# Kernel tuning notes

Measured on AMD Instinct MI355X. Metric: run time of the kernel, lower is better.

## Reference

```python
import jax, jax.numpy as jnp
import numpy as np

N_HEAD = 16
MASK_NEG = -10000.0


def setup_inputs() -> dict:
    key = jax.random.key(0)
    k1, k2, k3 = jax.random.split(key, 3)
    B, S, D = 4, 2048, 1024
    x = jax.random.normal(k1, (B, S, D), dtype=jnp.float32)
    c_attn_w = jax.random.normal(k2, (D, 3 * D), dtype=jnp.float32) * 0.02
    c_attn_b = jnp.zeros((3 * D,), dtype=jnp.float32)
    c_proj_w = jax.random.normal(k3, (D, D), dtype=jnp.float32) * 0.02
    c_proj_b = jnp.zeros((D,), dtype=jnp.float32)
    return {"x": x, "c_attn_w": c_attn_w, "c_attn_b": c_attn_b,
            "c_proj_w": c_proj_w, "c_proj_b": c_proj_b}


def reference(x, c_attn_w, c_attn_b, c_proj_w, c_proj_b):
    B, S, D = x.shape
    H = N_HEAD
    Dh = D // H
    # fused QKV projection (Conv1D = x @ W + b)
    qkv = x @ c_attn_w + c_attn_b          # [B,S,3D]
    q, k, v = jnp.split(qkv, 3, axis=-1)   # each [B,S,D]
    # split heads -> [B,H,S,Dh]
    q = q.reshape(B, S, H, Dh).transpose(0, 2, 1, 3)
    k = k.reshape(B, S, H, Dh).transpose(0, 2, 1, 3)
    v = v.reshape(B, S, H, Dh).transpose(0, 2, 1, 3)
    # scores with scaling (scale=True)
    w = jnp.einsum('bhqd,bhkd->bhqk', q, k) / jnp.sqrt(jnp.float32(Dh))
    # multiplicative causal mask: w*b + -10000*(1-b)
    b = jnp.tril(jnp.ones((S, S), dtype=w.dtype))[None, None]  # [1,1,S,S]
    w = w * b + MASK_NEG * (1.0 - b)
    w = jax.nn.softmax(w, axis=-1)
    # dropout is identity at inference
    a = jnp.einsum('bhqk,bhkd->bhqd', w, v)  # [B,H,S,Dh]
    a = a.transpose(0, 2, 1, 3).reshape(B, S, D)  # merge heads
    out = a @ c_proj_w + c_proj_b
    return out
```

## Files before the change

kernel.cpp:

```cpp
#include <hip/hip_runtime.h>

typedef unsigned short u16;
typedef short bf16x8 __attribute__((ext_vector_type(8)));
typedef float f32x4 __attribute__((ext_vector_type(4)));
typedef unsigned int u32;
typedef u32 u32x4 __attribute__((ext_vector_type(4)));

#define B_ 4
#define S_ 2048
#define D_ 1024
#define H_ 16
#define DH_ 64
#define M_ 8192
#define SCL2E 0.1803368801111244f

__device__ __forceinline__ u16 f2b(float f) {
  union { float f; unsigned int u; } v; v.f = f;
  unsigned int u = v.u;
  unsigned int r = (u + 0x7FFFu + ((u >> 16) & 1u)) >> 16;
  return (u16)r;
}

__device__ __forceinline__ void gload16(const void* g, void* l) {
  __builtin_amdgcn_global_load_lds(
      (const __attribute__((address_space(1))) unsigned int*)g,
      (__attribute__((address_space(3))) unsigned int*)l,
      16, 0, 0);
}

__device__ __forceinline__ u32 cvt_pk_bf16(float lo, float hi) {
  u32 r;
  asm("v_cvt_pk_bf16_f32 %0, %1, %2" : "=v"(r) : "v"(lo), "v"(hi));
  return r;
}

struct __attribute__((aligned(8))) u16x4 { u16 x, y, z, w; };

__global__ __launch_bounds__(256) void prep_fused(
    const float* __restrict__ x, u16* __restrict__ xb,
    const float* __restrict__ w1, u16* __restrict__ w1t,
    const float* __restrict__ w2, u16* __restrict__ w2t) {
  __shared__ float tile[32][33];
  const int bid = blockIdx.x, t = threadIdx.x;

  if (bid < 2048) {
    const int n = M_ * D_;
    for (int i = (bid * 256 + t) * 4; i < n; i += 2048 * 256 * 4) {
      float4 v = *(const float4*)(x + i);
      u16x4 o; o.x = f2b(v.x); o.y = f2b(v.y); o.z = f2b(v.z); o.w = f2b(v.w);
      *(u16x4*)(xb + i) = o;
    }
    return;
  }

  const float* in;  u16* outp;  int R, C, bx, by;
  if (bid < 5120) {
    int rel = bid - 2048; bx = rel % 96; by = rel / 96;
    in = w1; outp = w1t; R = 1024; C = 3072;
  } else {
    int rel = bid - 5120; bx = rel % 32; by = rel / 32;
    in = w2; outp = w2t; R = 1024; C = 1024;
  }
  const int c0 = bx * 32, r0 = by * 32;
  const int tx = t & 31, ty = t >> 5;
#pragma unroll
  for (int j = 0; j < 32; j += 8)
    tile[ty + j][tx] = in[(size_t)(r0 + ty + j) * C + c0 + tx];
  __syncthreads();
#pragma unroll
  for (int j = 0; j < 32; j += 8)
    outp[(size_t)(c0 + ty + j) * R + r0 + tx] = f2b(tile[tx][ty + j]);
}

template <int MODE>
__global__ __launch_bounds__(256) void gemm_bt(
    const u16* __restrict__ A, const u16* __restrict__ BT,
    const float* __restrict__ bias, float* __restrict__ outf,
    u16* __restrict__ qb, u16* __restrict__ kb, u16* __restrict__ vtb,
    int Ncols, int Kdim) {
  __shared__ __attribute__((aligned(16))) u16 lsA[2][128 * 64];
  __shared__ __attribute__((aligned(16))) u16 lsB[2][128 * 64];
  const int t = threadIdx.x;
  const int lane = t & 63, w = t >> 6;
  const int lhi = lane >> 4, llo = lane & 15;

  const int gx = gridDim.x;
  const int lin = blockIdx.y * gx + blockIdx.x;
  const int nwg = gx * gridDim.y;
  const int sw = (lin & 7) * (nwg >> 3) + (lin >> 3);
  const int m0 = (sw / gx) * 128, n0 = (sw % gx) * 128;

  const int wr = (w >> 1) * 64, wc = (w & 1) * 64;

  const int r8 = lane >> 3;
  const int scolE = ((lane & 7) ^ r8) * 8;
  const int srow = w * 32 + r8;

  f32x4 acc[4][4] = {};
  const int nt = Kdim >> 6;

#define STAGE_G(buf, kk0)                                                        \
  _Pragma("unroll") for (int j = 0; j < 4; ++j) {                                \
    gload16(A + (size_t)(m0 + srow + j * 8) * Kdim + (kk0) + scolE,              \
            &lsA[buf][(w * 32 + j * 8) * 64]);                                   \
    gload16(BT + (size_t)(n0 + srow + j * 8) * Kdim + (kk0) + scolE,             \
            &lsB[buf][(w * 32 + j * 8) * 64]);                                   \
  }

  STAGE_G(0, 0)

  for (int tt = 0; tt < nt; ++tt) {
    const int cur = tt & 1;
    if (tt + 1 < nt) {
      STAGE_G(cur ^ 1, (tt + 1) << 6)
      asm volatile("s_waitcnt vmcnt(8)" ::: "memory");
    } else {
      asm volatile("s_waitcnt vmcnt(0)" ::: "memory");
    }
    __builtin_amdgcn_sched_barrier(0);
    __builtin_amdgcn_s_barrier();
    __builtin_amdgcn_sched_barrier(0);
#pragma unroll
    for (int kk = 0; kk < 2; ++kk) {
      bf16x8 af[4], bfr[4];
#pragma unroll
      for (int i = 0; i < 4; ++i) {
        int ra = wr + i * 16 + llo;
        af[i] = *(const bf16x8*)((const char*)&lsA[cur][ra * 64] +
                                 ((kk * 64 + lhi * 16) ^ ((ra & 7) << 4)));
        int rb = wc + i * 16 + llo;
        bfr[i] = *(const bf16x8*)((const char*)&lsB[cur][rb * 64] +
                                  ((kk * 64 + lhi * 16) ^ ((rb & 7) << 4)));
      }
#pragma unroll
      for (int mi = 0; mi < 4; ++mi)
#pragma unroll
        for (int ni = 0; ni < 4; ++ni)
          acc[mi][ni] = __builtin_amdgcn_mfma_f32_16x16x32_bf16(af[mi], bfr[ni], acc[mi][ni], 0, 0, 0);
    }
    __builtin_amdgcn_sched_barrier(0);
    __builtin_amdgcn_s_barrier();
  }
#undef STAGE_G

  if (MODE == 0) {
#pragma unroll
    for (int mi = 0; mi < 4; ++mi)
#pragma unroll
      for (int ni = 0; ni < 4; ++ni)
#pragma unroll
        for (int r = 0; r < 4; ++r) {
          int m = m0 + wr + mi * 16 + lhi * 4 + r;
          int n = n0 + wc + ni * 16 + llo;
          outf[(size_t)m * Ncols + n] = acc[mi][ni][r] + bias[n];
        }
  } else if (n0 < 1024) {
#pragma unroll
    for (int mi = 0; mi < 4; ++mi)
#pragma unroll
      for (int ni = 0; ni < 4; ++ni)
#pragma unroll
        for (int r = 0; r < 4; ++r) {
          int m = m0 + wr + mi * 16 + lhi * 4 + r;
          int n = n0 + wc + ni * 16 + llo;
          int bidx = m >> 11, s = m & 2047, hh = n >> 6, dh = n & 63;
          qb[((size_t)(bidx * 16 + hh) * 2048 + s) * 64 + dh] =
              f2b((acc[mi][ni][r] + bias[n]) * SCL2E);
        }
  } else if (n0 < 2048) {
#pragma unroll
    for (int mi = 0; mi < 4; ++mi)
#pragma unroll
      for (int ni = 0; ni < 4; ++ni)
#pragma unroll
        for (int r = 0; r < 4; ++r) {
          int m = m0 + wr + mi * 16 + lhi * 4 + r;
          int n2 = n0 - 1024 + wc + ni * 16 + llo;
          int bidx = m >> 11, s = m & 2047, hh = n2 >> 6, dh = n2 & 63;
          kb[((size_t)(bidx * 16 + hh) * 2048 + s) * 64 + dh] =
              f2b(acc[mi][ni][r] + bias[n0 + wc + ni * 16 + llo]);
        }
  } else {
#pragma unroll
    for (int mi = 0; mi < 4; ++mi)
#pragma unroll
      for (int ni = 0; ni < 4; ++ni)
#pragma unroll
        for (int r = 0; r < 4; ++r) {
          int m = m0 + wr + mi * 16 + lhi * 4 + r;
          int n2 = n0 - 2048 + wc + ni * 16 + llo;
          int bidx = m >> 11, s = m & 2047, hh = n2 >> 6, dh = n2 & 63;
          int col = (s & ~127) | ((s & 15) * 8 + ((s >> 4) & 7));
          vtb[((size_t)(bidx * 16 + hh) * 64 + dh) * 2048 + col] =
              f2b(acc[mi][ni][r] + bias[n0 + wc + ni * 16 + llo]);
        }
  }
}

__global__ __launch_bounds__(512) void attn128(
    const u16* __restrict__ Qb, const u16* __restrict__ Kb,
    const u16* __restrict__ VTb, u16* __restrict__ AO) {
  __shared__ __attribute__((aligned(16))) u16 kls[128 * 64];
  __shared__ __attribute__((aligned(16))) u16 vls[64 * 128];
  __shared__ __attribute__((aligned(16))) u16 pl[8][16][136];
  const int t = threadIdx.x, w = t >> 6, lane = t & 63;
  const int lhi = lane >> 4, llo = lane & 15;

  const int lin = blockIdx.y * 8 + blockIdx.x;
  const int bh = ((lin >> 6) << 3) | (lin & 7);
  const int pr = (lin >> 3) & 7;
  const int bb = bh >> 4, hh = bh & 15;

  const u16* Qp = Qb + (size_t)bh * (S_ * DH_);
  const u16* Kp = Kb + (size_t)bh * (S_ * DH_);
  const u16* Vp = VTb + (size_t)bh * (DH_ * S_);

  bf16x8 ones;
#pragma unroll
  for (int i = 0; i < 8; ++i) ones[i] = (short)0x3F80;

  int krow[2], kcolE[2], kdst[2], vrow[2], vcolE[2], vdst[2];
#pragma unroll
  for (int c = 0; c < 2; ++c) {
    int b = c * 8192 + t * 16;
    krow[c] = b >> 7;
    kcolE[c] = (b & 127) >> 1;
    kdst[c] = krow[c] * 128 + ((b & 127) ^ ((krow[c] & 7) << 4));
    vrow[c] = b >> 8;
    vcolE[c] = (b & 255) >> 1;
    vdst[c] = vrow[c] * 256 + ((b & 255) ^ ((vrow[c] & 15) << 4));
  }

  for (int ci = 0; ci < 2; ++ci) {
    const int qc = ci ? (15 - pr) : pr;
    const int q0 = qc * 128;
    const int qrow = q0 + w * 16 + llo;
    bf16x8 aq0 = *(const bf16x8*)(Qp + (size_t)qrow * DH_ + lhi * 8);
    bf16x8 aq1 = *(const bf16x8*)(Qp + (size_t)qrow * DH_ + 32 + lhi * 8);
    const int n128 = qc + 1;

    bf16x8 kst[2], vst[2];
#pragma unroll
    for (int c = 0; c < 2; ++c) {
      kst[c] = *(const bf16x8*)(Kp + (size_t)krow[c] * DH_ + kcolE[c]);
      vst[c] = *(const bf16x8*)(Vp + (size_t)vrow[c] * S_ + vcolE[c]);
    }
    __syncthreads();
#pragma unroll
    for (int c = 0; c < 2; ++c) {
      *(bf16x8*)((char*)kls + kdst[c]) = kst[c];
      *(bf16x8*)((char*)vls + vdst[c]) = vst[c];
    }
    __syncthreads();

    f32x4 o[4] = {};
    f32x4 osum = {};
    const int crow = q0 + w * 16 + lhi * 4;
    const int sw = (llo & 7) << 4;

    for (int tt = 0; tt < n128 - 1; ++tt) {
      const int kv0 = tt << 7;
#pragma unroll
      for (int c = 0; c < 2; ++c) {
        kst[c] = *(const bf16x8*)(Kp + (size_t)(kv0 + 128 + krow[c]) * DH_ + kcolE[c]);
        vst[c] = *(const bf16x8*)(Vp + (size_t)vrow[c] * S_ + kv0 + 128 + vcolE[c]);
      }

      f32x4 sc[8] = {};
      __builtin_amdgcn_s_setprio(1);
#pragma unroll
      for (int f = 0; f < 8; ++f) {
        const char* base = (const char*)kls + (f * 16 + llo) * 128;
        bf16x8 bk0 = *(const bf16x8*)(base + ((lhi * 16) ^ sw));
        bf16x8 bk1 = *(const bf16x8*)(base + ((64 + lhi * 16) ^ sw));
        sc[f] = __builtin_amdgcn_mfma_f32_16x16x32_bf16(aq0, bk0, sc[f], 0, 0, 0);
        sc[f] = __builtin_amdgcn_mfma_f32_16x16x32_bf16(aq1, bk1, sc[f], 0, 0, 0);
      }
      __builtin_amdgcn_s_setprio(0);

#pragma unroll
      for (int r = 0; r < 4; ++r) {
        float p[8];
#pragma unroll
        for (int f = 0; f < 8; ++f) p[f] = exp2f(sc[f][r]);
        u32x4 pw;
        pw[0] = cvt_pk_bf16(p[0], p[1]);
        pw[1] = cvt_pk_bf16(p[2], p[3]);
        pw[2] = cvt_pk_bf16(p[4], p[5]);
        pw[3] = cvt_pk_bf16(p[6], p[7]);
        *(u32x4*)((char*)&pl[w][lhi * 4 + r][0] + llo * 16) = pw;
      }

      __builtin_amdgcn_s_setprio(1);
#pragma unroll
      for (int kk = 0; kk < 4; ++kk) {
        bf16x8 ap = *(const bf16x8*)((const char*)&pl[w][llo][0] + kk * 64 + lhi * 16);
#pragma unroll
        for (int f = 0; f < 4; ++f) {
          const char* vbase = (const char*)vls + (f * 16 + llo) * 256;
          bf16x8 bv = *(const bf16x8*)(vbase + ((kk * 64 + lhi * 16) ^ (llo << 4)));
          o[f] = __builtin_amdgcn_mfma_f32_16x16x32_bf16(ap, bv, o[f], 0, 0, 0);
        }
        osum = __builtin_amdgcn_mfma_f32_16x16x32_bf16(ap, ones, osum, 0, 0, 0);
      }
      __builtin_amdgcn_s_setprio(0);

      __syncthreads();
#pragma unroll
      for (int c = 0; c < 2; ++c) {
        *(bf16x8*)((char*)kls + kdst[c]) = kst[c];
        *(bf16x8*)((char*)vls + vdst[c]) = vst[c];
      }
      __syncthreads();
    }

    {
      const int kv0 = (n128 - 1) << 7;
      f32x4 sc[8] = {};
      __builtin_amdgcn_s_setprio(1);
#pragma unroll
      for (int f = 0; f < 8; ++f) {
        const char* base = (const char*)kls + (f * 16 + llo) * 128;
        bf16x8 bk0 = *(const bf16x8*)(base + ((lhi * 16) ^ sw));
        bf16x8 bk1 = *(const bf16x8*)(base + ((64 + lhi * 16) ^ sw));
        sc[f] = __builtin_amdgcn_mfma_f32_16x16x32_bf16(aq0, bk0, sc[f], 0, 0, 0);
        sc[f] = __builtin_amdgcn_mfma_f32_16x16x32_bf16(aq1, bk1, sc[f], 0, 0, 0);
      }
      __builtin_amdgcn_s_setprio(0);

#pragma unroll
      for (int r = 0; r < 4; ++r) {
        float p[8];
#pragma unroll
        for (int f = 0; f < 8; ++f) {
          float x = sc[f][r];
          if (kv0 + f * 16 + llo > crow + r) x = -1e30f;
          p[f] = exp2f(x);
        }
        u32x4 pw;
        pw[0] = cvt_pk_bf16(p[0], p[1]);
        pw[1] = cvt_pk_bf16(p[2], p[3]);
        pw[2] = cvt_pk_bf16(p[4], p[5]);
        pw[3] = cvt_pk_bf16(p[6], p[7]);
        *(u32x4*)((char*)&pl[w][lhi * 4 + r][0] + llo * 16) = pw;
      }

      __builtin_amdgcn_s_setprio(1);
#pragma unroll
      for (int kk = 0; kk < 4; ++kk) {
        bf16x8 ap = *(const bf16x8*)((const char*)&pl[w][llo][0] + kk * 64 + lhi * 16);
#pragma unroll
        for (int f = 0; f < 4; ++f) {
          const char* vbase = (const char*)vls + (f * 16 + llo) * 256;
          bf16x8 bv = *(const bf16x8*)(vbase + ((kk * 64 + lhi * 16) ^ (llo << 4)));
          o[f] = __builtin_amdgcn_mfma_f32_16x16x32_bf16(ap, bv, o[f], 0, 0, 0);
        }
        osum = __builtin_amdgcn_mfma_f32_16x16x32_bf16(ap, ones, osum, 0, 0, 0);
      }
      __builtin_amdgcn_s_setprio(0);
    }

#pragma unroll
    for (int f = 0; f < 4; ++f)
#pragma unroll
      for (int r = 0; r < 4; ++r) {
        int row = crow + r;
        int dh = f * 16 + llo;
        float val = o[f][r] / osum[r];
        AO[((size_t)bb * S_ + row) * D_ + hh * DH_ + dh] = f2b(val);
      }
  }
}

extern "C" void kernel_launch(void* const* d_in, const int* in_sizes, int n_in,
                              void* d_out, int out_size, void* d_ws, size_t ws_size,
                              hipStream_t stream) {
  const float* x  = (const float*)d_in[0];
  const float* w1 = (const float*)d_in[1];
  const float* b1 = (const float*)d_in[2];
  const float* w2 = (const float*)d_in[3];
  const float* b2 = (const float*)d_in[4];
  float* out = (float*)d_out;
  char* ws = (char*)d_ws;

  u16* xb  = (u16*)(ws);
  u16* w1t = (u16*)(ws + 16777216);
  u16* w2t = (u16*)(ws + 23068672);
  u16* qb  = (u16*)(ws + 25165824);
  u16* kb  = (u16*)(ws + 41943040);
  u16* vtb = (u16*)(ws + 58720256);
  u16* ao  = xb;

  prep_fused<<<6144, 256, 0, stream>>>(x, xb, w1, w1t, w2, w2t);

  gemm_bt<1><<<dim3(24, 64), 256, 0, stream>>>(xb, w1t, b1, nullptr, qb, kb, vtb, 3072, 1024);
  attn128<<<dim3(8, 64), 512, 0, stream>>>(qb, kb, vtb, ao);
  gemm_bt<0><<<dim3(8, 64), 256, 0, stream>>>(ao, w2t, b2, out, nullptr, nullptr, nullptr, 1024, 1024);
}
```

Before: 182.4 us.

## Stage K/V into LDS via direct global-to-LDS loads with pre-swizzled global layout

The QKV GEMM epilogue now writes K and V^T in an XOR-swizzled order, so the attention kernel can copy tiles straight into LDS with global_load_lds instead of staging them through registers. K gets a double buffer so the next tile's load is issued right after the score MFMAs. The P scratch buffer loses its padding and uses an XOR swizzle instead, and exp2f is replaced by raw v_exp_f32. This removes register staging and VGPR pressure, but V is still single-buffered behind a barrier and v_exp_f32 skips denormal handling.

```diff
diff --git a/kernel.cpp b/kernel.cpp
--- a/kernel.cpp
+++ b/kernel.cpp
@@ -31,6 +31,12 @@
 __device__ __forceinline__ u32 cvt_pk_bf16(float lo, float hi) {
   u32 r;
   asm("v_cvt_pk_bf16_f32 %0, %1, %2" : "=v"(r) : "v"(lo), "v"(hi));
+  return r;
+}
+
+__device__ __forceinline__ float fexp2(float x) {
+  float r;
+  asm("v_exp_f32 %0, %1" : "=v"(r) : "v"(x));
   return r;
 }
 
@@ -176,7 +182,8 @@
         for (int r = 0; r < 4; ++r) {
           int m = m0 + wr + mi * 16 + lhi * 4 + r;
           int n2 = n0 - 1024 + wc + ni * 16 + llo;
-          int bidx = m >> 11, s = m & 2047, hh = n2 >> 6, dh = n2 & 63;
+          int bidx = m >> 11, s = m & 2047, hh = n2 >> 6;
+          int dh = (n2 & 63) ^ ((s & 7) << 3);
           kb[((size_t)(bidx * 16 + hh) * 2048 + s) * 64 + dh] =
               f2b(acc[mi][ni][r] + bias[n0 + wc + ni * 16 + llo]);
         }
@@ -190,7 +197,8 @@
           int m = m0 + wr + mi * 16 + lhi * 4 + r;
           int n2 = n0 - 2048 + wc + ni * 16 + llo;
           int bidx = m >> 11, s = m & 2047, hh = n2 >> 6, dh = n2 & 63;
-          int col = (s & ~127) | ((s & 15) * 8 + ((s >> 4) & 7));
+          int slot = (s & 15) * 8 + ((s >> 4) & 7);
+          int col = (s & ~127) | (slot ^ ((dh & 15) << 3));
           vtb[((size_t)(bidx * 16 + hh) * 64 + dh) * 2048 + col] =
               f2b(acc[mi][ni][r] + bias[n0 + wc + ni * 16 + llo]);
         }
@@ -200,9 +208,9 @@
 __global__ __launch_bounds__(512) void attn128(
     const u16* __restrict__ Qb, const u16* __restrict__ Kb,
     const u16* __restrict__ VTb, u16* __restrict__ AO) {
-  __shared__ __attribute__((aligned(16))) u16 kls[128 * 64];
+  __shared__ __attribute__((aligned(16))) u16 kls[2][128 * 64];
   __shared__ __attribute__((aligned(16))) u16 vls[64 * 128];
-  __shared__ __attribute__((aligned(16))) u16 pl[8][16][136];
+  __shared__ __attribute__((aligned(16))) u16 pl[8][16][128];
   const int t = threadIdx.x, w = t >> 6, lane = t & 63;
   const int lhi = lane >> 4, llo = lane & 15;
 
@@ -219,17 +227,15 @@
 #pragma unroll
   for (int i = 0; i < 8; ++i) ones[i] = (short)0x3F80;
 
-  int krow[2], kcolE[2], kdst[2], vrow[2], vcolE[2], vdst[2];
-#pragma unroll
-  for (int c = 0; c < 2; ++c) {
-    int b = c * 8192 + t * 16;
-    krow[c] = b >> 7;
-    kcolE[c] = (b & 127) >> 1;
-    kdst[c] = krow[c] * 128 + ((b & 127) ^ ((krow[c] & 7) << 4));
-    vrow[c] = b >> 8;
-    vcolE[c] = (b & 255) >> 1;
-    vdst[c] = vrow[c] * 256 + ((b & 255) ^ ((vrow[c] & 15) << 4));
-  }
+#define STAGE_K(buf, kv0) {                                           \
+    const u16* s_ = Kp + (size_t)(kv0) * 64 + t * 8;                  \
+    gload16(s_,        &kls[buf][w * 512]);                           \
+    gload16(s_ + 4096, &kls[buf][4096 + w * 512]); }
+#define STAGE_V(kv0) {                                                \
+    gload16(Vp + (size_t)(t >> 4) * S_ + (kv0) + (t & 15) * 8,        \
+            &vls[w * 512]);                                           \
+    gload16(Vp + (size_t)(32 + (t >> 4)) * S_ + (kv0) + (t & 15) * 8, \
+            &vls[4096 + w * 512]); }
 
   for (int ci = 0; ci < 2; ++ci) {
     const int qc = ci ? (15 - pr) : pr;
@@ -239,18 +245,9 @@
     bf16x8 aq1 = *(const bf16x8*)(Qp + (size_t)qrow * DH_ + 32 + lhi * 8);
     const int n128 = qc + 1;
 
-    bf16x8 kst[2], vst[2];
-#pragma unroll
-    for (int c = 0; c < 2; ++c) {
-      kst[c] = *(const bf16x8*)(Kp + (size_t)krow[c] * DH_ + kcolE[c]);
-      vst[c] = *(const bf16x8*)(Vp + (size_t)vrow[c] * S_ + vcolE[c]);
-    }
     __syncthreads();
-#pragma unroll
-    for (int c = 0; c < 2; ++c) {
-      *(bf16x8*)((char*)kls + kdst[c]) = kst[c];
-      *(bf16x8*)((char*)vls + vdst[c]) = vst[c];
-    }
+    STAGE_K(0, 0)
+    STAGE_V(0)
     __syncthreads();
 
     f32x4 o[4] = {};
@@ -260,17 +257,13 @@
 
     for (int tt = 0; tt < n128 - 1; ++tt) {
       const int kv0 = tt << 7;
-#pragma unroll
-      for (int c = 0; c < 2; ++c) {
-        kst[c] = *(const bf16x8*)(Kp + (size_t)(kv0 + 128 + krow[c]) * DH_ + kcolE[c]);
-        vst[c] = *(const bf16x8*)(Vp + (size_t)vrow[c] * S_ + kv0 + 128 + vcolE[c]);
-      }
+      const int cur = tt & 1;
 
       f32x4 sc[8] = {};
       __builtin_amdgcn_s_setprio(1);
 #pragma unroll
       for (int f = 0; f < 8; ++f) {
-        const char* base = (const char*)kls + (f * 16 + llo) * 128;
+        const char* base = (const char*)&kls[cur][0] + (f * 16 + llo) * 128;
         bf16x8 bk0 = *(const bf16x8*)(base + ((lhi * 16) ^ sw));
         bf16x8 bk1 = *(const bf16x8*)(base + ((64 + lhi * 16) ^ sw));
         sc[f] = __builtin_amdgcn_mfma_f32_16x16x32_bf16(aq0, bk0, sc[f], 0, 0, 0);
@@ -278,23 +271,27 @@
       }
       __builtin_amdgcn_s_setprio(0);
 
+      STAGE_K(cur ^ 1, kv0 + 128)
+
 #pragma unroll
       for (int r = 0; r < 4; ++r) {
         float p[8];
 #pragma unroll
-        for (int f = 0; f < 8; ++f) p[f] = exp2f(sc[f][r]);
+        for (int f = 0; f < 8; ++f) p[f] = fexp2(sc[f][r]);
         u32x4 pw;
         pw[0] = cvt_pk_bf16(p[0], p[1]);
         pw[1] = cvt_pk_bf16(p[2], p[3]);
         pw[2] = cvt_pk_bf16(p[4], p[5]);
         pw[3] = cvt_pk_bf16(p[6], p[7]);
-        *(u32x4*)((char*)&pl[w][lhi * 4 + r][0] + llo * 16) = pw;
+        const int row = lhi * 4 + r;
+        *(u32x4*)((char*)&pl[w][0][0] + row * 256 + ((llo * 16) ^ ((row & 7) << 4))) = pw;
       }
 
       __builtin_amdgcn_s_setprio(1);
 #pragma unroll
       for (int kk = 0; kk < 4; ++kk) {
-        bf16x8 ap = *(const bf16x8*)((const char*)&pl[w][llo][0] + kk * 64 + lhi * 16);
+        bf16x8 ap = *(const bf16x8*)((const char*)&pl[w][0][0] + llo * 256 +
+                                     ((kk * 64 + lhi * 16) ^ ((llo & 7) << 4)));
 #pragma unroll
         for (int f = 0; f < 4; ++f) {
           const char* vbase = (const char*)vls + (f * 16 + llo) * 256;
@@ -306,21 +303,18 @@
       __builtin_amdgcn_s_setprio(0);
 
       __syncthreads();
-#pragma unroll
-      for (int c = 0; c < 2; ++c) {
-        *(bf16x8*)((char*)kls + kdst[c]) = kst[c];
-        *(bf16x8*)((char*)vls + vdst[c]) = vst[c];
-      }
+      STAGE_V(kv0 + 128)
       __syncthreads();
     }
 
     {
       const int kv0 = (n128 - 1) << 7;
+      const int cur = (n128 - 1) & 1;
       f32x4 sc[8] = {};
       __builtin_amdgcn_s_setprio(1);
 #pragma unroll
       for (int f = 0; f < 8; ++f) {
-        const char* base = (const char*)kls + (f * 16 + llo) * 128;
+        const char* base = (const char*)&kls[cur][0] + (f * 16 + llo) * 128;
         bf16x8 bk0 = *(const bf16x8*)(base + ((lhi * 16) ^ sw));
         bf16x8 bk1 = *(const bf16x8*)(base + ((64 + lhi * 16) ^ sw));
         sc[f] = __builtin_amdgcn_mfma_f32_16x16x32_bf16(aq0, bk0, sc[f], 0, 0, 0);
@@ -335,20 +329,22 @@
         for (int f = 0; f < 8; ++f) {
           float x = sc[f][r];
           if (kv0 + f * 16 + llo > crow + r) x = -1e30f;
-          p[f] = exp2f(x);
+          p[f] = fexp2(x);
         }
         u32x4 pw;
         pw[0] = cvt_pk_bf16(p[0], p[1]);
         pw[1] = cvt_pk_bf16(p[2], p[3]);
         pw[2] = cvt_pk_bf16(p[4], p[5]);
         pw[3] = cvt_pk_bf16(p[6], p[7]);
-        *(u32x4*)((char*)&pl[w][lhi * 4 + r][0] + llo * 16) = pw;
+        const int row = lhi * 4 + r;
+        *(u32x4*)((char*)&pl[w][0][0] + row * 256 + ((llo * 16) ^ ((row & 7) << 4))) = pw;
       }
 
       __builtin_amdgcn_s_setprio(1);
 #pragma unroll
       for (int kk = 0; kk < 4; ++kk) {
-        bf16x8 ap = *(const bf16x8*)((const char*)&pl[w][llo][0] + kk * 64 + lhi * 16);
+        bf16x8 ap = *(const bf16x8*)((const char*)&pl[w][0][0] + llo * 256 +
+                                     ((kk * 64 + lhi * 16) ^ ((llo & 7) << 4)));
 #pragma unroll
         for (int f = 0; f < 4; ++f) {
           const char* vbase = (const char*)vls + (f * 16 + llo) * 256;
@@ -370,6 +366,8 @@
         AO[((size_t)bb * S_ + row) * D_ + hh * DH_ + dh] = f2b(val);
       }
   }
+#undef STAGE_K
+#undef STAGE_V
 }
 
 extern "C" void kernel_launch(void* const* d_in, const int* in_sizes, int n_in,
```

Measured after the change: 185.1 us. Within noise of the previous version (+1.5%).
